# Performance work log

Hardware: AMD Instinct MI355X
Metric: run time of the kernel (lower is better)

The kernel has to match this reference:

```python
import jax, jax.numpy as jnp
import numpy as np

D_MODEL = 1024
NUM_HEADS = 16
D_K = D_MODEL // NUM_HEADS
THETA = 10000.0
SEQ = 4096
BATCH = 1


def _rope(x, token_positions):
    # x: [b, h, s, d_k]; interleaved even/odd rotation as in the torch module
    kd = jnp.arange(0, D_K, 2, dtype=jnp.float32) / D_K          # [d_k/2]
    angles = token_positions[:, None].astype(jnp.float32) / (THETA ** kd)  # [s, d_k/2]
    cos_pos = jnp.cos(angles)
    sin_pos = jnp.sin(angles)
    x_even = x[..., 0::2]
    x_odd = x[..., 1::2]
    rot_even = x_even * cos_pos - x_odd * sin_pos
    rot_odd = x_even * sin_pos + x_odd * cos_pos
    rot = jnp.stack([rot_even, rot_odd], axis=-1)                # [..., d_k/2, 2]
    return rot.reshape(*x.shape[:-1], D_K)


def setup_inputs() -> dict:
    key = jax.random.key(0)
    k1, k2, k3 = jax.random.split(key, 3)
    std_qkv = np.sqrt(2.0 / (D_MODEL + 3 * D_MODEL))
    std_o = np.sqrt(2.0 / (D_MODEL + D_MODEL))
    x = jax.random.normal(k1, (BATCH, SEQ, D_MODEL), dtype=jnp.float32)
    Wqkv = jax.random.normal(k2, (3 * D_MODEL, D_MODEL), dtype=jnp.float32) * std_qkv
    Wo = jax.random.normal(k3, (D_MODEL, D_MODEL), dtype=jnp.float32) * std_o
    token_positions = jnp.arange(SEQ, dtype=jnp.int32)
    return {"x": x, "Wqkv": Wqkv, "Wo": Wo, "token_positions": token_positions}


def reference(x, Wqkv, Wo, token_positions):
    b, s, _ = x.shape
    qkv = jnp.einsum('bsd,ed->bse', x, Wqkv)                      # [b, s, 3*d_model]
    q, k, v = jnp.split(qkv, 3, axis=-1)

    def to_heads(t):
        return t.reshape(b, s, NUM_HEADS, D_K).transpose(0, 2, 1, 3)  # [b, h, s, d_k]

    q, k, v = to_heads(q), to_heads(k), to_heads(v)
    q = _rope(q, token_positions)
    k = _rope(k, token_positions)

    scores = jnp.einsum('bhqd,bhkd->bhqk', q, k) / jnp.sqrt(jnp.float32(D_K))
    mask = jnp.tril(jnp.ones((s, s), dtype=bool))
    scores = jnp.where(mask, scores, -jnp.inf)
    attn = jax.nn.softmax(scores, axis=-1)
    out = jnp.einsum('bhqk,bhkd->bhqd', attn, v)                  # [b, h, s, d_k]
    out = out.transpose(0, 2, 1, 3).reshape(b, s, D_MODEL)
    return jnp.einsum('bsd,ed->bse', out, Wo)
```

## Files before the change

kernel.cpp:

```cpp
#include <hip/hip_runtime.h>
#include <cstdint>

typedef unsigned short u16;
typedef __attribute__((ext_vector_type(8))) short short8;
typedef __attribute__((ext_vector_type(4))) float float4v;

__device__ __forceinline__ float bf2f(u16 u) {
    union { unsigned int i; float f; } v; v.i = ((unsigned int)u) << 16; return v.f;
}
__device__ __forceinline__ u16 f2bf(float f) {
    union { float f; unsigned int i; } v; v.f = f;
    unsigned int i = v.i;
    i += 0x7fffu + ((i >> 16) & 1u);
    return (u16)(i >> 16);
}
__device__ __forceinline__ unsigned cvt_pk_bf16(float lo, float hi) {
    unsigned r;
    asm("v_cvt_pk_bf16_f32 %0, %1, %2" : "=v"(r) : "v"(lo), "v"(hi));
    return r;
}
__device__ __forceinline__ void gl2lds16(const u16* g, u16* l) {
    __builtin_amdgcn_global_load_lds((const __attribute__((address_space(1))) void*)g,
                                     (__attribute__((address_space(3))) void*)l, 16, 0, 0);
}
__device__ __forceinline__ uint4 cvt8(const float* __restrict__ p) {
    float4 a = *(const float4*)p;
    float4 b = *(const float4*)(p + 4);
    u16 t[8] = {f2bf(a.x), f2bf(a.y), f2bf(a.z), f2bf(a.w),
                f2bf(b.x), f2bf(b.y), f2bf(b.z), f2bf(b.w)};
    return *(const uint4*)t;
}

__global__ void cvt_xw(const float* __restrict__ x, const float* __restrict__ wq,
                       u16* __restrict__ xb, u16* __restrict__ wqb) {
    int i = blockIdx.x * blockDim.x + threadIdx.x;
    if (i < 524288) {
        *(uint4*)(xb + (size_t)i * 8) = cvt8(x + (size_t)i * 8);
    } else {
        int j = i - 524288;
        *(uint4*)(wqb + (size_t)j * 8) = cvt8(wq + (size_t)j * 8);
    }
}

__global__ void zero_cvt(float* __restrict__ acc, float* __restrict__ lac,
                         const float* __restrict__ wo, u16* __restrict__ wob) {
    int i = blockIdx.x * blockDim.x + threadIdx.x;
    float4 z = {0.f, 0.f, 0.f, 0.f};
    if (i < 1048576) {
        *(float4*)(acc + (size_t)i * 4) = z;
    } else if (i < 1064960) {
        *(float4*)(lac + (size_t)(i - 1048576) * 4) = z;
    } else {
        int j = i - 1064960;
        *(uint4*)(wob + (size_t)j * 8) = cvt8(wo + (size_t)j * 8);
    }
}

__global__ __launch_bounds__(256) void gemm_qkv(const u16* __restrict__ A,
                                                const u16* __restrict__ B,
                                                u16* __restrict__ C,
                                                const int* __restrict__ pos) {
    __shared__ u16 As[128 * 32];
    __shared__ u16 Bs[128 * 32];
    const int tid  = threadIdx.x;
    const int wave = tid >> 6, lane = tid & 63;
    const int lg = lane >> 4, lr = lane & 15;
    const int bm = blockIdx.x * 128, bn = blockIdx.y * 128;
    const int wm = (wave & 1) * 64, wn = (wave >> 1) * 64;
    const int row = tid >> 2, co = (tid & 3) * 8;

    float4v acc[4][4] = {};

    for (int k0 = 0; k0 < 1024; k0 += 32) {
        gl2lds16(A + (size_t)(bm + row) * 1024 + k0 + co,      As + tid * 8);
        gl2lds16(A + (size_t)(bm + 64 + row) * 1024 + k0 + co, As + (tid + 256) * 8);
        gl2lds16(B + (size_t)(bn + row) * 1024 + k0 + co,      Bs + tid * 8);
        gl2lds16(B + (size_t)(bn + 64 + row) * 1024 + k0 + co, Bs + (tid + 256) * 8);
        __syncthreads();

        short8 af[4], bf[4];
        #pragma unroll
        for (int i = 0; i < 4; ++i)
            af[i] = *(const short8*)(As + (wm + i * 16 + lr) * 32 + lg * 8);
        #pragma unroll
        for (int j = 0; j < 4; ++j)
            bf[j] = *(const short8*)(Bs + (wn + j * 16 + lr) * 32 + lg * 8);
        #pragma unroll
        for (int i = 0; i < 4; ++i)
            #pragma unroll
            for (int j = 0; j < 4; ++j)
                acc[i][j] = __builtin_amdgcn_mfma_f32_16x16x32_bf16(af[i], bf[j], acc[i][j], 0, 0, 0);
        __syncthreads();
    }

    const int colbase = bn + wn;
    const bool dorope = colbase < 2048;
    const float qsc = (colbase < 1024) ? 0.18033688011112042f : 1.0f;
    float freqs[4];
    if (dorope) {
        #pragma unroll
        for (int j = 0; j < 4; ++j)
            freqs[j] = __expf(-(float)((j * 16 + lr) >> 1) * 0.2878231366242557f);
    }
    #pragma unroll
    for (int i = 0; i < 4; ++i)
        #pragma unroll
        for (int r = 0; r < 4; ++r) {
            const int rw = bm + wm + i * 16 + lg * 4 + r;
            const float pr = dorope ? (float)pos[rw] : 0.f;
            #pragma unroll
            for (int j = 0; j < 4; ++j) {
                float v = acc[i][j][r];
                if (dorope) {
                    float sn, cs;
                    __sincosf(pr * freqs[j], &sn, &cs);
                    float p = __shfl_xor(v, 1);
                    float rot = (lr & 1) ? (p * sn + v * cs)
                                         : (v * cs - p * sn);
                    v = rot * qsc;
                }
                C[(size_t)rw * 3072 + colbase + j * 16 + lr] = f2bf(v);
            }
        }
}

__global__ __launch_bounds__(256) void transpose_v(const u16* __restrict__ qkv,
                                                   u16* __restrict__ VT) {
    __shared__ u16 T[64 * 65];
    const int h = blockIdx.y, s0 = blockIdx.x * 64;
    const int tid = threadIdx.x;
    #pragma unroll
    for (int i = 0; i < 2; ++i) {
        int seg = i * 256 + tid;
        int r = seg >> 3, c8 = (seg & 7) * 8;
        u16 tmp[8];
        *(uint4*)tmp = *(const uint4*)(qkv + (size_t)(s0 + r) * 3072 + 2048 + h * 64 + c8);
        #pragma unroll
        for (int j = 0; j < 8; ++j) T[r * 65 + c8 + j] = tmp[j];
    }
    __syncthreads();
    #pragma unroll
    for (int i = 0; i < 2; ++i) {
        int seg = i * 256 + tid;
        int d = seg >> 3, s8 = (seg & 7) * 8;
        u16 tmp[8];
        #pragma unroll
        for (int j = 0; j < 8; ++j) tmp[j] = T[(s8 + j) * 65 + d];
        *(uint4*)(VT + (size_t)(h * 64 + d) * 4096 + s0 + s8) = *(const uint4*)tmp;
    }
}

__device__ __forceinline__ void attn_tile(const u16* __restrict__ Ksub,
                                          const u16* __restrict__ Vsub,
                                          u16* __restrict__ Psw,
                                          int tbase, int qrow0, int q_abs,
                                          int lg, int lr, int swz,
                                          const short8 qf[2], float4v o_acc[4], float& rs) {
    float4v sc[4];
    #pragma unroll
    for (int jt = 0; jt < 4; ++jt) {
        float4v a = {};
        #pragma unroll
        for (int kk = 0; kk < 2; ++kk) {
            short8 kf = *(const short8*)(Ksub + (jt * 16 + lr) * 64 + (((kk * 4 + lg) ^ swz) * 8));
            a = __builtin_amdgcn_mfma_f32_16x16x32_bf16(kf, qf[kk], a, 0, 0, 0);
        }
        sc[jt] = a;
    }
    const bool mk = (tbase + 63 > qrow0);
    #pragma unroll
    for (int jt = 0; jt < 4; ++jt) {
        float e[4];
        #pragma unroll
        for (int r = 0; r < 4; ++r) {
            float s = sc[jt][r];
            if (mk && (tbase + jt * 16 + lg * 4 + r > q_abs)) s = -30000.f;
            e[r] = __builtin_amdgcn_exp2f(fminf(s, 86.562f));
        }
        rs += (e[0] + e[1]) + (e[2] + e[3]);
        uint2 w;
        w.x = cvt_pk_bf16(e[0], e[1]);
        w.y = cvt_pk_bf16(e[2], e[3]);
        *(uint2*)(Psw + lr * 72 + jt * 16 + lg * 4) = w;
    }
    short8 pf[2];
    #pragma unroll
    for (int kk = 0; kk < 2; ++kk)
        pf[kk] = *(const short8*)(Psw + lr * 72 + kk * 32 + lg * 8);
    #pragma unroll
    for (int jd = 0; jd < 4; ++jd) {
        float4v a = o_acc[jd];
        #pragma unroll
        for (int kk = 0; kk < 2; ++kk) {
            short8 vf = *(const short8*)(Vsub + (jd * 16 + lr) * 64 + (((kk * 4 + lg) ^ swz) * 8));
            a = __builtin_amdgcn_mfma_f32_16x16x32_bf16(pf[kk], vf, a, 0, 0, 0);
        }
        o_acc[jd] = a;
    }
}

__global__ __launch_bounds__(512) void attn_kernel(const u16* __restrict__ qkv,
                                                   const u16* __restrict__ VT,
                                                   float* __restrict__ acc,
                                                   float* __restrict__ lac) {
    __shared__ u16 Ks[2 * 64 * 64];
    __shared__ u16 Vt[2 * 64 * 64];
    __shared__ u16 Ps[8][16 * 72];

    const int tid  = threadIdx.x;
    const int wave = tid >> 6, lane = tid & 63;
    const int lg = lane >> 4, lr = lane & 15;
    const int h  = blockIdx.y;
    const int z  = blockIdx.z;

    const int srow = tid >> 3;
    const int sg   = tid & 7;
    const int sco  = sg * 8;
    const int sldso = srow * 64 + ((sg ^ (srow & 7)) * 8);
    const int swz = (lr & 7);

    const u16* Kgbase = qkv + (size_t)srow * 3072 + 1024 + h * 64 + sco;
    const u16* Vgbase = VT + (size_t)(h * 64 + srow) * 4096 + sco;

    #pragma unroll 1
    for (int part = 0; part < 2; ++part) {
        const int qt = part ? (31 - (int)blockIdx.x) : (int)blockIdx.x;
        const int qb = qt * 128;
        const int qrow0 = qb + wave * 16;
        const int q_abs = qrow0 + lr;
        const int tmax = qb + 64;
        const int t0s  = z * 64;

        short8 qf[2];
        #pragma unroll
        for (int kk = 0; kk < 2; ++kk)
            qf[kk] = *(const short8*)(qkv + (size_t)(qrow0 + lr) * 3072 + h * 64 + kk * 32 + lg * 8);

        float4v o_acc[4] = {};
        float rs = 0.f;

        uint4 rK0 = *(const uint4*)(Kgbase + (size_t)t0s * 3072);
        uint4 rV0 = *(const uint4*)(Vgbase + t0s);
        const bool pB = (t0s + 128 <= tmax);
        uint4 rK1, rV1;
        if (pB) {
            rK1 = *(const uint4*)(Kgbase + (size_t)(t0s + 128) * 3072);
            rV1 = *(const uint4*)(Vgbase + t0s + 128);
        }
        __syncthreads();
        *(uint4*)(Ks + sldso) = rK0;
        *(uint4*)(Vt + sldso) = rV0;
        if (pB) {
            *(uint4*)(Ks + 4096 + sldso) = rK1;
            *(uint4*)(Vt + 4096 + sldso) = rV1;
        }
        __syncthreads();

        for (int t0 = t0s; t0 <= tmax; t0 += 256) {
            const bool hasB  = (t0 + 128 <= tmax);
            const bool hasN  = (t0 + 256 <= tmax);
            const bool hasNB = (t0 + 384 <= tmax);
            if (hasN) {
                rK0 = *(const uint4*)(Kgbase + (size_t)(t0 + 256) * 3072);
                rV0 = *(const uint4*)(Vgbase + t0 + 256);
            }
            if (hasNB) {
                rK1 = *(const uint4*)(Kgbase + (size_t)(t0 + 384) * 3072);
                rV1 = *(const uint4*)(Vgbase + t0 + 384);
            }

            attn_tile(Ks, Vt, Ps[wave], t0, qrow0, q_abs, lg, lr, swz, qf, o_acc, rs);
            if (hasB)
                attn_tile(Ks + 4096, Vt + 4096, Ps[wave], t0 + 128, qrow0, q_abs,
                          lg, lr, swz, qf, o_acc, rs);

            if (hasN) {
                __syncthreads();
                *(uint4*)(Ks + sldso) = rK0;
                *(uint4*)(Vt + sldso) = rV0;
                if (hasNB) {
                    *(uint4*)(Ks + 4096 + sldso) = rK1;
                    *(uint4*)(Vt + 4096 + sldso) = rV1;
                }
                __syncthreads();
            }
        }

        float t = rs;
        t += __shfl_xor(t, 16, 64);
        t += __shfl_xor(t, 32, 64);
        if (lane < 16)
            atomicAdd(&lac[(size_t)(qrow0 + lr) * 16 + h], t);

        #pragma unroll
        for (int jd = 0; jd < 4; ++jd)
            #pragma unroll
            for (int r = 0; r < 4; ++r) {
                int s = qrow0 + lg * 4 + r;
                int d = jd * 16 + lr;
                atomicAdd(&acc[(size_t)s * 1024 + h * 64 + d], o_acc[jd][r]);
            }
    }
}

__global__ void norm_o(const float* __restrict__ acc, const float* __restrict__ lac,
                       u16* __restrict__ qkv, float* __restrict__ outp) {
    int i = blockIdx.x * blockDim.x + threadIdx.x;
    if (i < 524288) {
        int e0 = i * 8;
        int s = e0 >> 10, c = e0 & 1023, h = c >> 6;
        float inv = 1.0f / lac[(size_t)s * 16 + h];
        float4 a = *(const float4*)(acc + e0);
        float4 b = *(const float4*)(acc + e0 + 4);
        u16 t[8] = {f2bf(a.x * inv), f2bf(a.y * inv), f2bf(a.z * inv), f2bf(a.w * inv),
                    f2bf(b.x * inv), f2bf(b.y * inv), f2bf(b.z * inv), f2bf(b.w * inv)};
        *(uint4*)(qkv + (size_t)s * 3072 + c) = *(const uint4*)t;
    } else {
        int j = i - 524288;
        float4 z = {0.f, 0.f, 0.f, 0.f};
        *(float4*)(outp + (size_t)j * 4) = z;
    }
}

__global__ __launch_bounds__(256) void gemm_oproj(const u16* __restrict__ A,
                                                  const u16* __restrict__ B,
                                                  float* __restrict__ C) {
    __shared__ u16 As[128 * 32];
    __shared__ u16 Bs[128 * 32];
    const int tid  = threadIdx.x;
    const int wave = tid >> 6, lane = tid & 63;
    const int lg = lane >> 4, lr = lane & 15;
    const int bm = blockIdx.x * 128, bn = blockIdx.y * 128;
    const int wm = (wave & 1) * 64, wn = (wave >> 1) * 64;
    const int row = tid >> 2, co = (tid & 3) * 8;
    const int kbase = blockIdx.z * 512;

    float4v acc[4][4] = {};

    for (int k0 = kbase; k0 < kbase + 512; k0 += 32) {
        gl2lds16(A + (size_t)(bm + row) * 3072 + k0 + co,      As + tid * 8);
        gl2lds16(A + (size_t)(bm + 64 + row) * 3072 + k0 + co, As + (tid + 256) * 8);
        gl2lds16(B + (size_t)(bn + row) * 1024 + k0 + co,      Bs + tid * 8);
        gl2lds16(B + (size_t)(bn + 64 + row) * 1024 + k0 + co, Bs + (tid + 256) * 8);
        __syncthreads();

        short8 af[4], bf[4];
        #pragma unroll
        for (int i = 0; i < 4; ++i)
            af[i] = *(const short8*)(As + (wm + i * 16 + lr) * 32 + lg * 8);
        #pragma unroll
        for (int j = 0; j < 4; ++j)
            bf[j] = *(const short8*)(Bs + (wn + j * 16 + lr) * 32 + lg * 8);
        #pragma unroll
        for (int i = 0; i < 4; ++i)
            #pragma unroll
            for (int j = 0; j < 4; ++j)
                acc[i][j] = __builtin_amdgcn_mfma_f32_16x16x32_bf16(af[i], bf[j], acc[i][j], 0, 0, 0);
        __syncthreads();
    }

    #pragma unroll
    for (int i = 0; i < 4; ++i)
        #pragma unroll
        for (int j = 0; j < 4; ++j)
            #pragma unroll
            for (int r = 0; r < 4; ++r) {
                int rw = bm + wm + i * 16 + lg * 4 + r;
                int cl = bn + wn + j * 16 + lr;
                atomicAdd(&C[(size_t)rw * 1024 + cl], acc[i][j][r]);
            }
}

__global__ void fill_diag(float* __restrict__ p, size_t n, float mark) {
    size_t i = (size_t)blockIdx.x * blockDim.x + threadIdx.x;
    if (i < n) p[i] = 0.f;
    if (i == 0) p[0] = mark;
}

extern "C" void kernel_launch(void* const* d_in, const int* in_sizes, int n_in,
                              void* d_out, int out_size, void* d_ws, size_t ws_size,
                              hipStream_t stream) {
    int ix = -1, iwq = -1, iwo = -1, ip = -1;
    for (int i = 0; i < n_in; ++i) {
        if      (in_sizes[i] == 4096 * 1024) ix = i;
        else if (in_sizes[i] == 3072 * 1024) iwq = i;
        else if (in_sizes[i] == 1024 * 1024) iwo = i;
        else if (in_sizes[i] == 4096)        ip = i;
    }
    float* out = (float*)d_out;
    const size_t OUT_E = (size_t)4096 * 1024;
    const size_t QKV_E = (size_t)4096 * 3072;
    const size_t NEED  = QKV_E * 2 + (size_t)3072 * 1024 * 2;

    if (ix < 0 || iwq < 0 || iwo < 0 || ip < 0 || out_size != (int)OUT_E) {
        fill_diag<<<(int)((OUT_E + 255) / 256), 256, 0, stream>>>(out, OUT_E, 1000.0f);
        return;
    }
    if (ws_size < NEED) {
        fill_diag<<<(int)((OUT_E + 255) / 256), 256, 0, stream>>>(out, OUT_E, 500.0f);
        return;
    }
    const float* x    = (const float*)d_in[ix];
    const float* Wqkv = (const float*)d_in[iwq];
    const float* Wo   = (const float*)d_in[iwo];
    const int*   pos  = (const int*)d_in[ip];

    u16* qkv   = (u16*)d_ws;
    u16* wq_bf = (u16*)d_ws + QKV_E;
    u16* wo_bf = wq_bf;
    float* lac = (float*)((char*)wq_bf + 2 * 1024 * 1024 + 65536);
    u16* x_bf  = (u16*)d_out;
    u16* VT    = (u16*)d_out + OUT_E;
    float* acc = (float*)d_in[ix];

    cvt_xw<<<3584, 256, 0, stream>>>(x, Wqkv, x_bf, wq_bf);
    gemm_qkv<<<dim3(32, 24), 256, 0, stream>>>(x_bf, wq_bf, qkv, pos);
    zero_cvt<<<4672, 256, 0, stream>>>(acc, lac, Wo, wo_bf);
    transpose_v<<<dim3(64, 16), 256, 0, stream>>>(qkv, VT);
    attn_kernel<<<dim3(16, 16, 2), 512, 0, stream>>>(qkv, VT, acc, lac);
    norm_o<<<6144, 256, 0, stream>>>(acc, lac, qkv, out);
    gemm_oproj<<<dim3(32, 8, 2), 256, 0, stream>>>(qkv, wo_bf, out);
}
```

Before: 260.6 us.

## Precompute RoPE table, merge prep kernels, drop split-K atomics in output projection

RoPE cos/sin values are now precomputed once into a table inside the conversion kernel, so the QKV GEMM epilogue no longer calls sincos and exp per element. The V transpose and the zero/Wo-conversion kernels are merged into one launch. The output projection switches from split-K with float atomics into a pre-zeroed output to a full-K GEMM with 128x64 tiles and plain stores, which also removes the output zeroing in norm_o. The cost is an extra table read in the epilogue and a longer K loop per block in the projection.

```diff
diff --git a/kernel.cpp b/kernel.cpp
--- a/kernel.cpp
+++ b/kernel.cpp
@@ -32,34 +32,31 @@
 }
 
 __global__ void cvt_xw(const float* __restrict__ x, const float* __restrict__ wq,
-                       u16* __restrict__ xb, u16* __restrict__ wqb) {
+                       const int* __restrict__ pos,
+                       u16* __restrict__ xb, u16* __restrict__ wqb,
+                       float2* __restrict__ tb) {
     int i = blockIdx.x * blockDim.x + threadIdx.x;
     if (i < 524288) {
         *(uint4*)(xb + (size_t)i * 8) = cvt8(x + (size_t)i * 8);
-    } else {
+    } else if (i < 917504) {
         int j = i - 524288;
         *(uint4*)(wqb + (size_t)j * 8) = cvt8(wq + (size_t)j * 8);
-    }
-}
-
-__global__ void zero_cvt(float* __restrict__ acc, float* __restrict__ lac,
-                         const float* __restrict__ wo, u16* __restrict__ wob) {
-    int i = blockIdx.x * blockDim.x + threadIdx.x;
-    float4 z = {0.f, 0.f, 0.f, 0.f};
-    if (i < 1048576) {
-        *(float4*)(acc + (size_t)i * 4) = z;
-    } else if (i < 1064960) {
-        *(float4*)(lac + (size_t)(i - 1048576) * 4) = z;
     } else {
-        int j = i - 1064960;
-        *(uint4*)(wob + (size_t)j * 8) = cvt8(wo + (size_t)j * 8);
+        int j = i - 917504;
+        int s = j >> 5, f = j & 31;
+        float freq = __expf(-(float)f * 0.2878231366242557f);
+        float ang  = (float)pos[s] * freq;
+        float sn, cs;
+        __sincosf(ang, &sn, &cs);
+        float2 t; t.x = cs; t.y = sn;
+        tb[j] = t;
     }
 }
 
 __global__ __launch_bounds__(256) void gemm_qkv(const u16* __restrict__ A,
                                                 const u16* __restrict__ B,
                                                 u16* __restrict__ C,
-                                                const int* __restrict__ pos) {
+                                                const float2* __restrict__ tb) {
     __shared__ u16 As[128 * 32];
     __shared__ u16 Bs[128 * 32];
     const int tid  = threadIdx.x;
@@ -96,27 +93,19 @@
     const int colbase = bn + wn;
     const bool dorope = colbase < 2048;
     const float qsc = (colbase < 1024) ? 0.18033688011112042f : 1.0f;
-    float freqs[4];
-    if (dorope) {
-        #pragma unroll
-        for (int j = 0; j < 4; ++j)
-            freqs[j] = __expf(-(float)((j * 16 + lr) >> 1) * 0.2878231366242557f);
-    }
     #pragma unroll
     for (int i = 0; i < 4; ++i)
         #pragma unroll
         for (int r = 0; r < 4; ++r) {
             const int rw = bm + wm + i * 16 + lg * 4 + r;
-            const float pr = dorope ? (float)pos[rw] : 0.f;
             #pragma unroll
             for (int j = 0; j < 4; ++j) {
                 float v = acc[i][j][r];
                 if (dorope) {
-                    float sn, cs;
-                    __sincosf(pr * freqs[j], &sn, &cs);
+                    float2 t = tb[rw * 32 + ((j * 16 + lr) >> 1)];
                     float p = __shfl_xor(v, 1);
-                    float rot = (lr & 1) ? (p * sn + v * cs)
-                                         : (v * cs - p * sn);
+                    float rot = (lr & 1) ? (p * t.y + v * t.x)
+                                         : (v * t.x - p * t.y);
                     v = rot * qsc;
                 }
                 C[(size_t)rw * 3072 + colbase + j * 16 + lr] = f2bf(v);
@@ -124,29 +113,47 @@
         }
 }
 
-__global__ __launch_bounds__(256) void transpose_v(const u16* __restrict__ qkv,
-                                                   u16* __restrict__ VT) {
+__global__ __launch_bounds__(256) void prep2(const u16* __restrict__ qkv,
+                                             u16* __restrict__ VT,
+                                             float* __restrict__ acc,
+                                             float* __restrict__ lac,
+                                             const float* __restrict__ wo,
+                                             u16* __restrict__ wob) {
     __shared__ u16 T[64 * 65];
-    const int h = blockIdx.y, s0 = blockIdx.x * 64;
+    const int bid = blockIdx.x;
     const int tid = threadIdx.x;
-    #pragma unroll
-    for (int i = 0; i < 2; ++i) {
-        int seg = i * 256 + tid;
-        int r = seg >> 3, c8 = (seg & 7) * 8;
-        u16 tmp[8];
-        *(uint4*)tmp = *(const uint4*)(qkv + (size_t)(s0 + r) * 3072 + 2048 + h * 64 + c8);
-        #pragma unroll
-        for (int j = 0; j < 8; ++j) T[r * 65 + c8 + j] = tmp[j];
-    }
-    __syncthreads();
-    #pragma unroll
-    for (int i = 0; i < 2; ++i) {
-        int seg = i * 256 + tid;
-        int d = seg >> 3, s8 = (seg & 7) * 8;
-        u16 tmp[8];
-        #pragma unroll
-        for (int j = 0; j < 8; ++j) tmp[j] = T[(s8 + j) * 65 + d];
-        *(uint4*)(VT + (size_t)(h * 64 + d) * 4096 + s0 + s8) = *(const uint4*)tmp;
+    if (bid < 1024) {
+        const int h = bid >> 6, s0 = (bid & 63) * 64;
+        #pragma unroll
+        for (int i = 0; i < 2; ++i) {
+            int seg = i * 256 + tid;
+            int r = seg >> 3, c8 = (seg & 7) * 8;
+            u16 tmp[8];
+            *(uint4*)tmp = *(const uint4*)(qkv + (size_t)(s0 + r) * 3072 + 2048 + h * 64 + c8);
+            #pragma unroll
+            for (int j = 0; j < 8; ++j) T[r * 65 + c8 + j] = tmp[j];
+        }
+        __syncthreads();
+        #pragma unroll
+        for (int i = 0; i < 2; ++i) {
+            int seg = i * 256 + tid;
+            int d = seg >> 3, s8 = (seg & 7) * 8;
+            u16 tmp[8];
+            #pragma unroll
+            for (int j = 0; j < 8; ++j) tmp[j] = T[(s8 + j) * 65 + d];
+            *(uint4*)(VT + (size_t)(h * 64 + d) * 4096 + s0 + s8) = *(const uint4*)tmp;
+        }
+    } else {
+        int i = (bid - 1024) * 256 + tid;
+        float4 z = {0.f, 0.f, 0.f, 0.f};
+        if (i < 1048576) {
+            *(float4*)(acc + (size_t)i * 4) = z;
+        } else if (i < 1064960) {
+            *(float4*)(lac + (size_t)(i - 1048576) * 4) = z;
+        } else {
+            int j = i - 1064960;
+            *(uint4*)(wob + (size_t)j * 8) = cvt8(wo + (size_t)j * 8);
+        }
     }
 }
 
@@ -304,57 +311,51 @@
 }
 
 __global__ void norm_o(const float* __restrict__ acc, const float* __restrict__ lac,
-                       u16* __restrict__ qkv, float* __restrict__ outp) {
+                       u16* __restrict__ qkv) {
     int i = blockIdx.x * blockDim.x + threadIdx.x;
-    if (i < 524288) {
-        int e0 = i * 8;
-        int s = e0 >> 10, c = e0 & 1023, h = c >> 6;
-        float inv = 1.0f / lac[(size_t)s * 16 + h];
-        float4 a = *(const float4*)(acc + e0);
-        float4 b = *(const float4*)(acc + e0 + 4);
-        u16 t[8] = {f2bf(a.x * inv), f2bf(a.y * inv), f2bf(a.z * inv), f2bf(a.w * inv),
-                    f2bf(b.x * inv), f2bf(b.y * inv), f2bf(b.z * inv), f2bf(b.w * inv)};
-        *(uint4*)(qkv + (size_t)s * 3072 + c) = *(const uint4*)t;
-    } else {
-        int j = i - 524288;
-        float4 z = {0.f, 0.f, 0.f, 0.f};
-        *(float4*)(outp + (size_t)j * 4) = z;
-    }
+    if (i >= 4096 * 1024 / 8) return;
+    int e0 = i * 8;
+    int s = e0 >> 10, c = e0 & 1023, h = c >> 6;
+    float inv = 1.0f / lac[(size_t)s * 16 + h];
+    float4 a = *(const float4*)(acc + e0);
+    float4 b = *(const float4*)(acc + e0 + 4);
+    u16 t[8] = {f2bf(a.x * inv), f2bf(a.y * inv), f2bf(a.z * inv), f2bf(a.w * inv),
+                f2bf(b.x * inv), f2bf(b.y * inv), f2bf(b.z * inv), f2bf(b.w * inv)};
+    *(uint4*)(qkv + (size_t)s * 3072 + c) = *(const uint4*)t;
 }
 
 __global__ __launch_bounds__(256) void gemm_oproj(const u16* __restrict__ A,
                                                   const u16* __restrict__ B,
                                                   float* __restrict__ C) {
     __shared__ u16 As[128 * 32];
-    __shared__ u16 Bs[128 * 32];
+    __shared__ u16 Bs[64 * 32];
     const int tid  = threadIdx.x;
     const int wave = tid >> 6, lane = tid & 63;
     const int lg = lane >> 4, lr = lane & 15;
-    const int bm = blockIdx.x * 128, bn = blockIdx.y * 128;
-    const int wm = (wave & 1) * 64, wn = (wave >> 1) * 64;
+    const int bm = blockIdx.x * 128, bn = blockIdx.y * 64;
+    const int wm = (wave & 1) * 64, wn = (wave >> 1) * 32;
     const int row = tid >> 2, co = (tid & 3) * 8;
-    const int kbase = blockIdx.z * 512;
-
-    float4v acc[4][4] = {};
-
-    for (int k0 = kbase; k0 < kbase + 512; k0 += 32) {
+
+    float4v acc[4][2] = {};
+
+    for (int k0 = 0; k0 < 1024; k0 += 32) {
         gl2lds16(A + (size_t)(bm + row) * 3072 + k0 + co,      As + tid * 8);
         gl2lds16(A + (size_t)(bm + 64 + row) * 3072 + k0 + co, As + (tid + 256) * 8);
-        gl2lds16(B + (size_t)(bn + row) * 1024 + k0 + co,      Bs + tid * 8);
-        gl2lds16(B + (size_t)(bn + 64 + row) * 1024 + k0 + co, Bs + (tid + 256) * 8);
-        __syncthreads();
-
-        short8 af[4], bf[4];
+        if (row < 64)
+            gl2lds16(B + (size_t)(bn + row) * 1024 + k0 + co,  Bs + tid * 8);
+        __syncthreads();
+
+        short8 af[4], bf[2];
         #pragma unroll
         for (int i = 0; i < 4; ++i)
             af[i] = *(const short8*)(As + (wm + i * 16 + lr) * 32 + lg * 8);
         #pragma unroll
-        for (int j = 0; j < 4; ++j)
+        for (int j = 0; j < 2; ++j)
             bf[j] = *(const short8*)(Bs + (wn + j * 16 + lr) * 32 + lg * 8);
         #pragma unroll
         for (int i = 0; i < 4; ++i)
             #pragma unroll
-            for (int j = 0; j < 4; ++j)
+            for (int j = 0; j < 2; ++j)
                 acc[i][j] = __builtin_amdgcn_mfma_f32_16x16x32_bf16(af[i], bf[j], acc[i][j], 0, 0, 0);
         __syncthreads();
     }
@@ -362,12 +363,12 @@
     #pragma unroll
     for (int i = 0; i < 4; ++i)
         #pragma unroll
-        for (int j = 0; j < 4; ++j)
+        for (int j = 0; j < 2; ++j)
             #pragma unroll
             for (int r = 0; r < 4; ++r) {
                 int rw = bm + wm + i * 16 + lg * 4 + r;
                 int cl = bn + wn + j * 16 + lr;
-                atomicAdd(&C[(size_t)rw * 1024 + cl], acc[i][j][r]);
+                C[(size_t)rw * 1024 + cl] = acc[i][j][r];
             }
 }
 
@@ -411,13 +412,13 @@
     float* lac = (float*)((char*)wq_bf + 2 * 1024 * 1024 + 65536);
     u16* x_bf  = (u16*)d_out;
     u16* VT    = (u16*)d_out + OUT_E;
+    float2* tb = (float2*)VT;
     float* acc = (float*)d_in[ix];
 
-    cvt_xw<<<3584, 256, 0, stream>>>(x, Wqkv, x_bf, wq_bf);
-    gemm_qkv<<<dim3(32, 24), 256, 0, stream>>>(x_bf, wq_bf, qkv, pos);
-    zero_cvt<<<4672, 256, 0, stream>>>(acc, lac, Wo, wo_bf);
-    transpose_v<<<dim3(64, 16), 256, 0, stream>>>(qkv, VT);
+    cvt_xw<<<4096, 256, 0, stream>>>(x, Wqkv, pos, x_bf, wq_bf, tb);
+    gemm_qkv<<<dim3(32, 24), 256, 0, stream>>>(x_bf, wq_bf, qkv, tb);
+    prep2<<<5696, 256, 0, stream>>>(qkv, VT, acc, lac, Wo, wo_bf);
     attn_kernel<<<dim3(16, 16, 2), 512, 0, stream>>>(qkv, VT, acc, lac);
-    norm_o<<<6144, 256, 0, stream>>>(acc, lac, qkv, out);
-    gemm_oproj<<<dim3(32, 8, 2), 256, 0, stream>>>(qkv, wo_bf, out);
-}
+    norm_o<<<2048, 256, 0, stream>>>(acc, lac, qkv);
+    gemm_oproj<<<dim3(32, 16), 256, 0, stream>>>(qkv, wo_bf, out);
+}
```

Result: faster. 243.1 us (-6.7%).
